# Kernel tuning notes

Measured on AMD Instinct MI355X. Metric: run time of the kernel, lower is better.

The kernel has to match this reference:

```python
import jax, jax.numpy as jnp
import numpy as np

SEQ, B, I, H = 1000, 1, 900, 4096

def setup_inputs() -> dict:
    key = jax.random.key(0)
    k1, k2, k3, k4 = jax.random.split(key, 4)
    inputs = jax.random.normal(k1, (SEQ, B, I), dtype=jnp.float32)
    state = jnp.zeros((B, H), dtype=jnp.float32)
    W_ih = jax.random.normal(k2, (H, I), dtype=jnp.float32) * 0.1
    # scale recurrent weights so effective spectral radius ~0.9 (keeps tanh stable)
    W_hh = jax.random.normal(k3, (H, H), dtype=jnp.float32) * (0.9 / np.sqrt(H))
    W_out = jax.random.normal(k4, (I, H + I + 1), dtype=jnp.float32) * 0.02
    return {"inputs": inputs, "state": state, "W_ih": W_ih, "W_hh": W_hh, "W_out": W_out}

def reference(inputs, state, W_ih, W_hh, W_out):
    """TorchESN._forward: per-step reservoir update + linear readout on [1, inp, state]."""
    ones = jnp.ones((1, 1), dtype=inputs.dtype)

    def step(s, inp):
        inp_flat = inp.reshape(1, -1)                       # (1, I)
        s = jnp.tanh(inp_flat @ W_ih.T + s @ W_hh.T)        # (1, H) ESN cell
        ext = jnp.concatenate([ones, inp_flat, s], axis=1)  # (1, 1+I+H)
        out = ext @ W_out.T                                  # (1, I)
        return s, (out, s)

    _, (outs, states) = jax.lax.scan(step, state, inputs)
    outputs = outs.reshape(inputs.shape)   # (seq, 1, I)
    states = states.squeeze(1)             # (seq, H)
    return outputs, states
```

## Files before the change

### kernel.cpp

```cpp
#include <hip/hip_runtime.h>
#include <hip/hip_fp16.h>

#define SEQ  1000
#define IDIM 900
#define H    4096

#define LDS_BYTES (16384 + 320)

typedef _Float16 h2_t __attribute__((ext_vector_type(2)));

__device__ __forceinline__ float fdot2(unsigned a, unsigned b, float c) {
#if __has_builtin(__builtin_amdgcn_fdot2)
    return __builtin_amdgcn_fdot2(__builtin_bit_cast(h2_t, a),
                                  __builtin_bit_cast(h2_t, b), c, false);
#else
    h2_t ha = __builtin_bit_cast(h2_t, a);
    h2_t hb = __builtin_bit_cast(h2_t, b);
    return c + (float)ha.x * (float)hb.x + (float)ha.y * (float)hb.y;
#endif
}

__device__ __forceinline__ float tanh_fast(float x) {
    float ax = __builtin_fabsf(x);
    float e  = __expf(-2.0f * ax);
    float t  = (1.0f - e) / (1.0f + e);
    return __builtin_copysignf(t, x);
}

__device__ __forceinline__ int swz2(int d) { return d ^ (((d >> 5) & 7) << 2); }

__device__ __forceinline__ uint4 pack8(float4 f0, float4 f1) {
    __half2 p; uint4 u;
    p = __floats2half2_rn(f0.x, f0.y); u.x = *(unsigned*)&p;
    p = __floats2half2_rn(f0.z, f0.w); u.y = *(unsigned*)&p;
    p = __floats2half2_rn(f1.x, f1.y); u.z = *(unsigned*)&p;
    p = __floats2half2_rn(f1.z, f1.w); u.w = *(unsigned*)&p;
    return u;
}

__global__ __launch_bounds__(1024, 4) void esn_recurrent(
    const float* __restrict__ Whh,
    const float* __restrict__ pre_in,
    float*       __restrict__ states,
    unsigned long long* __restrict__ part)
{
    extern __shared__ char smem[];
    unsigned* s2   = (unsigned*)smem;
    float*    redf = (float*)(smem + 16384);

    const int B    = blockIdx.x;
    const int tid  = threadIdx.x;
    const int wave = tid >> 6;
    const int lane = tid & 63;
    const int h    = wave >> 2;
    const int qd   = wave & 3;

    if (wave == 0) {
        float s0 = 0.f;
        if (lane < 16) {
            s0 = tanh_fast(pre_in[(B << 4) + lane]);
            states[(B << 4) + lane] = s0;
        }
        float a = __shfl(s0, lane << 1);
        float b = __shfl(s0, (lane << 1) + 1);
        if (lane < 8) {
            __half2 p = __floats2half2_rn(a, b);
            unsigned long long wrd = (1ull << 32)
                                   | (unsigned long long)(*(unsigned*)&p);
            __hip_atomic_store(part + (B << 3) + lane, wrd,
                               __ATOMIC_RELAXED, __HIP_MEMORY_SCOPE_AGENT);
        }
    }

    uint4 wa0, wb0, wa1, wb1, wa2, wb2, wa3, wb3;
    {
        const float* wsrc = Whh + ((size_t)((B << 4) + (h << 2))) * H
                          + (qd << 10) + (lane << 4);
        const float4* r0 = (const float4*)(wsrc);
        const float4* r1 = (const float4*)(wsrc + H);
        const float4* r2 = (const float4*)(wsrc + 2 * H);
        const float4* r3 = (const float4*)(wsrc + 3 * H);
        wa0 = pack8(r0[0], r0[1]); wb0 = pack8(r0[2], r0[3]);
        wa1 = pack8(r1[0], r1[1]); wb1 = pack8(r1[2], r1[3]);
        wa2 = pack8(r2[0], r2[1]); wb2 = pack8(r2[2], r2[3]);
        wa3 = pack8(r3[0], r3[1]); wb3 = pack8(r3[2], r3[3]);
    }

    for (int t = 0; t < SEQ - 1; ++t) {
        float pv = 0.f;
        if (tid < 16) pv = pre_in[(size_t)(t + 1) * H + (B << 4) + tid];

        {
            const unsigned long long* pb = part + ((size_t)(t & 3) << 11) + (tid << 1);
            const unsigned want = (unsigned)(t + 1);
            unsigned long long v0, v1;
            for (;;) {
                v0 = __hip_atomic_load(pb,     __ATOMIC_RELAXED, __HIP_MEMORY_SCOPE_AGENT);
                v1 = __hip_atomic_load(pb + 1, __ATOMIC_RELAXED, __HIP_MEMORY_SCOPE_AGENT);
                if ((unsigned)(v0 >> 32) == want && (unsigned)(v1 >> 32) == want) break;
                __builtin_amdgcn_s_sleep(1);
            }
            uint2 w; w.x = (unsigned)v0; w.y = (unsigned)v1;
            *(uint2*)(s2 + ((t & 1) << 11) + swz2(tid << 1)) = w;
        }
        __syncthreads();

        const unsigned* sb = s2 + ((t & 1) << 11);
        const int cb = (qd << 9) + (lane << 3);
        uint4 sa = *(const uint4*)(sb + swz2(cb));
        uint4 sc = *(const uint4*)(sb + swz2(cb + 4));

        float a0 = 0.f, a1 = 0.f, a2 = 0.f, a3 = 0.f;
        a0 = fdot2(wa0.x, sa.x, a0); a0 = fdot2(wa0.y, sa.y, a0);
        a0 = fdot2(wa0.z, sa.z, a0); a0 = fdot2(wa0.w, sa.w, a0);
        a0 = fdot2(wb0.x, sc.x, a0); a0 = fdot2(wb0.y, sc.y, a0);
        a0 = fdot2(wb0.z, sc.z, a0); a0 = fdot2(wb0.w, sc.w, a0);
        a1 = fdot2(wa1.x, sa.x, a1); a1 = fdot2(wa1.y, sa.y, a1);
        a1 = fdot2(wa1.z, sa.z, a1); a1 = fdot2(wa1.w, sa.w, a1);
        a1 = fdot2(wb1.x, sc.x, a1); a1 = fdot2(wb1.y, sc.y, a1);
        a1 = fdot2(wb1.z, sc.z, a1); a1 = fdot2(wb1.w, sc.w, a1);
        a2 = fdot2(wa2.x, sa.x, a2); a2 = fdot2(wa2.y, sa.y, a2);
        a2 = fdot2(wa2.z, sa.z, a2); a2 = fdot2(wa2.w, sa.w, a2);
        a2 = fdot2(wb2.x, sc.x, a2); a2 = fdot2(wb2.y, sc.y, a2);
        a2 = fdot2(wb2.z, sc.z, a2); a2 = fdot2(wb2.w, sc.w, a2);
        a3 = fdot2(wa3.x, sa.x, a3); a3 = fdot2(wa3.y, sa.y, a3);
        a3 = fdot2(wa3.z, sa.z, a3); a3 = fdot2(wa3.w, sa.w, a3);
        a3 = fdot2(wb3.x, sc.x, a3); a3 = fdot2(wb3.y, sc.y, a3);
        a3 = fdot2(wb3.z, sc.z, a3); a3 = fdot2(wb3.w, sc.w, a3);

        float y0 = (lane & 1) ? a0 : a1;
        float x  = (lane & 1) ? a1 : a0;
        x += __shfl_xor(y0, 1);
        float y1 = (lane & 1) ? a2 : a3;
        float z  = (lane & 1) ? a3 : a2;
        z += __shfl_xor(y1, 1);
        float y2 = (lane & 2) ? x : z;
        float u  = (lane & 2) ? z : x;
        u += __shfl_xor(y2, 2);
        u += __shfl_xor(u, 4);
        u += __shfl_xor(u, 8);
        u += __shfl_xor(u, 16);
        u += __shfl_xor(u, 32);

        if (lane < 4) redf[((h << 2) + lane) * 5 + qd] = u;
        __syncthreads();

        if (wave == 0) {
            float sf = 0.f;
            if (lane < 16) {
                const float* rf = redf + lane * 5;
                sf = tanh_fast(rf[0] + rf[1] + rf[2] + rf[3] + pv);
                states[(size_t)(t + 1) * H + (B << 4) + lane] = sf;
            }
            float a = __shfl(sf, lane << 1);
            float b = __shfl(sf, (lane << 1) + 1);
            if (lane < 8) {
                __half2 p = __floats2half2_rn(a, b);
                unsigned long long wrd = ((unsigned long long)(unsigned)(t + 2) << 32)
                                       | (unsigned long long)(*(unsigned*)&p);
                __hip_atomic_store(part + ((size_t)((t + 1) & 3) << 11) + (B << 3) + lane,
                                   wrd, __ATOMIC_RELAXED, __HIP_MEMORY_SCOPE_AGENT);
            }
        }
    }
}

#define BM 64
#define BN 64
#define BK 32

__global__ __launch_bounds__(256) void gemm_abt(
    const float* __restrict__ A, int lda,
    const float* __restrict__ B, int ldb,
    float*       __restrict__ C, int ldc,
    int Mdim, int N, int K, int mode,
    const float* __restrict__ X, const float* __restrict__ S)
{
    __shared__ __align__(16) float As[BK][BM + 4];
    __shared__ __align__(16) float Bs[BK][BN + 4];

    const int tid = threadIdx.x;
    const int n0  = blockIdx.x * BN;
    const int m0  = blockIdx.y * BM;
    const int tx  = tid & 15;
    const int ty  = tid >> 4;

    float c[4][4] = {};

    for (int k0 = 0; k0 < K; k0 += BK) {
        #pragma unroll
        for (int p = 0; p < 8; ++p) {
            const int idx = tid + p * 256;
            const int mm  = idx >> 5;
            const int kk  = idx & 31;
            const int gk  = k0 + kk;

            float av = 0.f;
            const int gm = m0 + mm;
            if (gm < Mdim && gk < K) {
                if (mode == 0) {
                    av = A[(size_t)gm * lda + gk];
                } else {
                    if (gk == 0)          av = 1.0f;
                    else if (gk <= IDIM)  av = X[(size_t)gm * IDIM + (gk - 1)];
                    else                  av = S[(size_t)gm * H + (gk - 1 - IDIM)];
                }
            }
            As[kk][mm] = av;

            float bv = 0.f;
            const int gn = n0 + mm;
            if (gn < N && gk < K) bv = B[(size_t)gn * ldb + gk];
            Bs[kk][mm] = bv;
        }
        __syncthreads();

        #pragma unroll
        for (int kk = 0; kk < BK; ++kk) {
            float4 a = *(const float4*)&As[kk][ty * 4];
            float4 b = *(const float4*)&Bs[kk][tx * 4];
            float av[4] = {a.x, a.y, a.z, a.w};
            float bv[4] = {b.x, b.y, b.z, b.w};
            #pragma unroll
            for (int i = 0; i < 4; ++i)
                #pragma unroll
                for (int j = 0; j < 4; ++j)
                    c[i][j] += av[i] * bv[j];
        }
        __syncthreads();
    }

    #pragma unroll
    for (int i = 0; i < 4; ++i) {
        const int gm = m0 + ty * 4 + i;
        if (gm >= Mdim) continue;
        #pragma unroll
        for (int j = 0; j < 4; ++j) {
            const int gn = n0 + tx * 4 + j;
            if (gn < N) C[(size_t)gm * ldc + gn] = c[i][j];
        }
    }
}

#define KSLICE 1280

__global__ __launch_bounds__(256) void gemm_splitk_h(
    const float* __restrict__ Bw, int ldb,
    float*       __restrict__ Cp,
    int Mdim, int N, int K,
    const float* __restrict__ X, const float* __restrict__ S)
{
    __shared__ __align__(16) unsigned As16[16][BM + 4];
    __shared__ __align__(16) unsigned Bs16[16][BN + 4];

    const int tid = threadIdx.x;
    const int n0  = blockIdx.x * BN;
    const int m0  = blockIdx.y * BM;
    const int z   = blockIdx.z;
    const int tx  = tid & 15;
    const int ty  = tid >> 4;

    const int kbeg = z * KSLICE;
    const int kend = min(K, kbeg + KSLICE);

    float c[4][4] = {};

    for (int k0 = kbeg; k0 < kend; k0 += BK) {
        const bool pureS = (k0 >= IDIM + 1) && (k0 + BK <= kend) && (k0 + BK <= K);
        const bool pureX = (k0 > 0) && (k0 + BK <= IDIM + 1);
        #pragma unroll
        for (int p = 0; p < 4; ++p) {
            const int idx = tid + p * 256;
            const int mm  = idx >> 4;
            const int kp  = idx & 15;
            const int gk  = k0 + (kp << 1);
            const int gm  = m0 + mm;

            float e0 = 0.f, e1 = 0.f;
            if (gm < Mdim) {
                if (pureS) {
                    const float* sp = S + (size_t)gm * H + (gk - 1 - IDIM);
                    e0 = sp[0]; e1 = sp[1];
                } else if (pureX) {
                    const float* xp = X + (size_t)gm * IDIM + (gk - 1);
                    e0 = xp[0]; e1 = xp[1];
                } else {
                    if (gk < kend) {
                        if (gk == 0)          e0 = 1.0f;
                        else if (gk <= IDIM)  e0 = X[(size_t)gm * IDIM + (gk - 1)];
                        else                  e0 = S[(size_t)gm * H + (gk - 1 - IDIM)];
                    }
                    const int g1 = gk + 1;
                    if (g1 < kend) {
                        if (g1 == 0)          e1 = 1.0f;
                        else if (g1 <= IDIM)  e1 = X[(size_t)gm * IDIM + (g1 - 1)];
                        else                  e1 = S[(size_t)gm * H + (g1 - 1 - IDIM)];
                    }
                }
            }
            __half2 ha = __floats2half2_rn(e0, e1);
            As16[kp][mm] = *(unsigned*)&ha;

            float b0 = 0.f, b1 = 0.f;
            const int gn = n0 + mm;
            if (gn < N) {
                if (gk < kend)     b0 = Bw[(size_t)gn * ldb + gk];
                if (gk + 1 < kend) b1 = Bw[(size_t)gn * ldb + gk + 1];
            }
            __half2 hb = __floats2half2_rn(b0, b1);
            Bs16[kp][mm] = *(unsigned*)&hb;
        }
        __syncthreads();

        #pragma unroll
        for (int kp = 0; kp < 16; ++kp) {
            uint4 ua = *(const uint4*)&As16[kp][ty * 4];
            uint4 ub = *(const uint4*)&Bs16[kp][tx * 4];
            unsigned av[4] = {ua.x, ua.y, ua.z, ua.w};
            unsigned bv[4] = {ub.x, ub.y, ub.z, ub.w};
            #pragma unroll
            for (int i = 0; i < 4; ++i)
                #pragma unroll
                for (int j = 0; j < 4; ++j)
                    c[i][j] = fdot2(av[i], bv[j], c[i][j]);
        }
        __syncthreads();
    }

    float* Cz = Cp + (size_t)z * ((size_t)SEQ * IDIM);
    #pragma unroll
    for (int i = 0; i < 4; ++i) {
        const int gm = m0 + ty * 4 + i;
        if (gm >= Mdim) continue;
        #pragma unroll
        for (int j = 0; j < 4; ++j) {
            const int gn = n0 + tx * 4 + j;
            if (gn < N) Cz[(size_t)gm * N + gn] = c[i][j];
        }
    }
}

__global__ __launch_bounds__(256) void reduce4(
    const float4* __restrict__ p, float4* __restrict__ o, int n4)
{
    const size_t stride = (size_t)SEQ * IDIM / 4;
    for (int i = blockIdx.x * 256 + threadIdx.x; i < n4; i += gridDim.x * 256) {
        float4 a = p[i];
        float4 b = p[i + stride];
        float4 c = p[i + 2 * stride];
        float4 d = p[i + 3 * stride];
        float4 r;
        r.x = a.x + b.x + c.x + d.x;
        r.y = a.y + b.y + c.y + d.y;
        r.z = a.z + b.z + c.z + d.z;
        r.w = a.w + b.w + c.w + d.w;
        o[i] = r;
    }
}

extern "C" void kernel_launch(void* const* d_in, const int* in_sizes, int n_in,
                              void* d_out, int out_size, void* d_ws, size_t ws_size,
                              hipStream_t stream) {
    const float* inputs = (const float*)d_in[0];
    const float* W_ih   = (const float*)d_in[2];
    const float* W_hh   = (const float*)d_in[3];
    const float* W_out  = (const float*)d_in[4];

    float* out    = (float*)d_out;
    float* states = out + (size_t)SEQ * IDIM;

    float* pre_in = (float*)d_ws;
    float* cpart  = pre_in + (size_t)SEQ * H;

    const size_t ws_needed = ((size_t)SEQ * H + 4ull * SEQ * IDIM) * sizeof(float);
    const bool   use_splitk = (ws_size >= ws_needed);

    unsigned long long* part = (unsigned long long*)out;

    (void)hipFuncSetAttribute((const void*)esn_recurrent,
                              hipFuncAttributeMaxDynamicSharedMemorySize,
                              LDS_BYTES);

    gemm_abt<<<dim3(H / BN, (SEQ + BM - 1) / BM), 256, 0, stream>>>(
        inputs, IDIM, W_ih, IDIM, pre_in, H, SEQ, H, IDIM, 0, nullptr, nullptr);

    {
        const float* whh_p = W_hh;
        const float* pin_p = pre_in;
        float* st_p = states;
        unsigned long long* part_p = part;
        void* args[] = { (void*)&whh_p, (void*)&pin_p, (void*)&st_p, (void*)&part_p };
        hipLaunchCooperativeKernel((const void*)esn_recurrent,
                                   dim3(256), dim3(1024), args, LDS_BYTES, stream);
    }

    if (use_splitk) {
        gemm_splitk_h<<<dim3((IDIM + BN - 1) / BN, (SEQ + BM - 1) / BM, 4),
                        256, 0, stream>>>(
            W_out, 1 + IDIM + H, cpart, SEQ, IDIM, 1 + IDIM + H, inputs, states);
        const int n4 = SEQ * IDIM / 4;
        reduce4<<<dim3(880), 256, 0, stream>>>(
            (const float4*)cpart, (float4*)out, n4);
    } else {
        gemm_abt<<<dim3((IDIM + BN - 1) / BN, (SEQ + BM - 1) / BM), 256, 0, stream>>>(
            nullptr, 0, W_out, 1 + IDIM + H, out, IDIM,
            SEQ, IDIM, 1 + IDIM + H, 1, inputs, states);
    }
}
```

Measured before the change: 3.536 ms.

## Fuse input projection into recurrent kernel with register-resident W_ih slices

Removes the separate GEMM that precomputed inputs@W_ih^T into a workspace buffer. Each thread of the persistent recurrent kernel now holds a float4 slice of W_ih in registers and computes the input contribution per step, folding it into the existing fdot2 accumulators and reduction. This saves a kernel launch and the pre_in write/read traffic. In exchange it adds register pressure and a per-step global load of the input row inside the serial loop, overlapped with the spin-wait.

Result: faster. 3.018 ms (-14.6%).

```diff
diff --git a/kernel.cpp b/kernel.cpp
--- a/kernel.cpp
+++ b/kernel.cpp
@@ -40,7 +40,8 @@
 
 __global__ __launch_bounds__(1024, 4) void esn_recurrent(
     const float* __restrict__ Whh,
-    const float* __restrict__ pre_in,
+    const float* __restrict__ Wih,
+    const float* __restrict__ X,
     float*       __restrict__ states,
     unsigned long long* __restrict__ part)
 {
@@ -55,22 +56,8 @@
     const int h    = wave >> 2;
     const int qd   = wave & 3;
 
-    if (wave == 0) {
-        float s0 = 0.f;
-        if (lane < 16) {
-            s0 = tanh_fast(pre_in[(B << 4) + lane]);
-            states[(B << 4) + lane] = s0;
-        }
-        float a = __shfl(s0, lane << 1);
-        float b = __shfl(s0, (lane << 1) + 1);
-        if (lane < 8) {
-            __half2 p = __floats2half2_rn(a, b);
-            unsigned long long wrd = (1ull << 32)
-                                   | (unsigned long long)(*(unsigned*)&p);
-            __hip_atomic_store(part + (B << 3) + lane, wrd,
-                               __ATOMIC_RELAXED, __HIP_MEMORY_SCOPE_AGENT);
-        }
-    }
+    const int c0   = ((qd << 6) + lane) << 2;
+    const bool sOK = (c0 < IDIM);
 
     uint4 wa0, wb0, wa1, wb1, wa2, wb2, wa3, wb3;
     {
@@ -85,10 +72,62 @@
         wa2 = pack8(r2[0], r2[1]); wb2 = pack8(r2[2], r2[3]);
         wa3 = pack8(r3[0], r3[1]); wb3 = pack8(r3[2], r3[3]);
     }
+    float4 wi0 = {}, wi1 = {}, wi2 = {}, wi3 = {};
+    if (sOK) {
+        const float* wis = Wih + (size_t)((B << 4) + (h << 2)) * IDIM + c0;
+        wi0 = *(const float4*)(wis);
+        wi1 = *(const float4*)(wis + IDIM);
+        wi2 = *(const float4*)(wis + 2 * IDIM);
+        wi3 = *(const float4*)(wis + 3 * IDIM);
+    }
+
+    {
+        float4 xv = {};
+        if (sOK) xv = *(const float4*)(X + c0);
+        float a0 = fmaf(wi0.w, xv.w, fmaf(wi0.z, xv.z, fmaf(wi0.y, xv.y, wi0.x * xv.x)));
+        float a1 = fmaf(wi1.w, xv.w, fmaf(wi1.z, xv.z, fmaf(wi1.y, xv.y, wi1.x * xv.x)));
+        float a2 = fmaf(wi2.w, xv.w, fmaf(wi2.z, xv.z, fmaf(wi2.y, xv.y, wi2.x * xv.x)));
+        float a3 = fmaf(wi3.w, xv.w, fmaf(wi3.z, xv.z, fmaf(wi3.y, xv.y, wi3.x * xv.x)));
+
+        float y0 = (lane & 1) ? a0 : a1;
+        float x  = (lane & 1) ? a1 : a0;
+        x += __shfl_xor(y0, 1);
+        float y1 = (lane & 1) ? a2 : a3;
+        float z  = (lane & 1) ? a3 : a2;
+        z += __shfl_xor(y1, 1);
+        float y2 = (lane & 2) ? x : z;
+        float u  = (lane & 2) ? z : x;
+        u += __shfl_xor(y2, 2);
+        u += __shfl_xor(u, 4);
+        u += __shfl_xor(u, 8);
+        u += __shfl_xor(u, 16);
+        u += __shfl_xor(u, 32);
+
+        if (lane < 4) redf[((h << 2) + lane) * 5 + qd] = u;
+        __syncthreads();
+
+        if (wave == 0) {
+            float sf = 0.f;
+            if (lane < 16) {
+                const float* rf = redf + lane * 5;
+                sf = tanh_fast(rf[0] + rf[1] + rf[2] + rf[3]);
+                states[(B << 4) + lane] = sf;
+            }
+            float a = __shfl(sf, lane << 1);
+            float b = __shfl(sf, (lane << 1) + 1);
+            if (lane < 8) {
+                __half2 p = __floats2half2_rn(a, b);
+                unsigned long long wrd = (1ull << 32)
+                                       | (unsigned long long)(*(unsigned*)&p);
+                __hip_atomic_store(part + (B << 3) + lane, wrd,
+                                   __ATOMIC_RELAXED, __HIP_MEMORY_SCOPE_AGENT);
+            }
+        }
+    }
 
     for (int t = 0; t < SEQ - 1; ++t) {
-        float pv = 0.f;
-        if (tid < 16) pv = pre_in[(size_t)(t + 1) * H + (B << 4) + tid];
+        float4 xv = {};
+        if (sOK) xv = *(const float4*)(X + (size_t)(t + 1) * IDIM + c0);
 
         {
             const unsigned long long* pb = part + ((size_t)(t & 3) << 11) + (tid << 1);
@@ -105,12 +144,16 @@
         }
         __syncthreads();
 
+        float a0 = fmaf(wi0.w, xv.w, fmaf(wi0.z, xv.z, fmaf(wi0.y, xv.y, wi0.x * xv.x)));
+        float a1 = fmaf(wi1.w, xv.w, fmaf(wi1.z, xv.z, fmaf(wi1.y, xv.y, wi1.x * xv.x)));
+        float a2 = fmaf(wi2.w, xv.w, fmaf(wi2.z, xv.z, fmaf(wi2.y, xv.y, wi2.x * xv.x)));
+        float a3 = fmaf(wi3.w, xv.w, fmaf(wi3.z, xv.z, fmaf(wi3.y, xv.y, wi3.x * xv.x)));
+
         const unsigned* sb = s2 + ((t & 1) << 11);
         const int cb = (qd << 9) + (lane << 3);
         uint4 sa = *(const uint4*)(sb + swz2(cb));
         uint4 sc = *(const uint4*)(sb + swz2(cb + 4));
 
-        float a0 = 0.f, a1 = 0.f, a2 = 0.f, a3 = 0.f;
         a0 = fdot2(wa0.x, sa.x, a0); a0 = fdot2(wa0.y, sa.y, a0);
         a0 = fdot2(wa0.z, sa.z, a0); a0 = fdot2(wa0.w, sa.w, a0);
         a0 = fdot2(wb0.x, sc.x, a0); a0 = fdot2(wb0.y, sc.y, a0);
@@ -149,7 +192,7 @@
             float sf = 0.f;
             if (lane < 16) {
                 const float* rf = redf + lane * 5;
-                sf = tanh_fast(rf[0] + rf[1] + rf[2] + rf[3] + pv);
+                sf = tanh_fast(rf[0] + rf[1] + rf[2] + rf[3]);
                 states[(size_t)(t + 1) * H + (B << 4) + lane] = sf;
             }
             float a = __shfl(sf, lane << 1);
@@ -369,10 +412,9 @@
     float* out    = (float*)d_out;
     float* states = out + (size_t)SEQ * IDIM;
 
-    float* pre_in = (float*)d_ws;
-    float* cpart  = pre_in + (size_t)SEQ * H;
-
-    const size_t ws_needed = ((size_t)SEQ * H + 4ull * SEQ * IDIM) * sizeof(float);
+    float* cpart  = (float*)d_ws;
+
+    const size_t ws_needed = 4ull * SEQ * IDIM * sizeof(float);
     const bool   use_splitk = (ws_size >= ws_needed);
 
     unsigned long long* part = (unsigned long long*)out;
@@ -381,15 +423,14 @@
                               hipFuncAttributeMaxDynamicSharedMemorySize,
                               LDS_BYTES);
 
-    gemm_abt<<<dim3(H / BN, (SEQ + BM - 1) / BM), 256, 0, stream>>>(
-        inputs, IDIM, W_ih, IDIM, pre_in, H, SEQ, H, IDIM, 0, nullptr, nullptr);
-
     {
         const float* whh_p = W_hh;
-        const float* pin_p = pre_in;
+        const float* wih_p = W_ih;
+        const float* x_p   = inputs;
         float* st_p = states;
         unsigned long long* part_p = part;
-        void* args[] = { (void*)&whh_p, (void*)&pin_p, (void*)&st_p, (void*)&part_p };
+        void* args[] = { (void*)&whh_p, (void*)&wih_p, (void*)&x_p,
+                         (void*)&st_p, (void*)&part_p };
         hipLaunchCooperativeKernel((const void*)esn_recurrent,
                                    dim3(256), dim3(1024), args, LDS_BYTES, stream);
     }
```
